# Kernel optimization log

Hardware: AMD Instinct MI355X
Metric: run time of the kernel (lower is better)

Reference implementation:

```python
import jax, jax.numpy as jnp
import numpy as np

B, S, D, H = 8, 512, 1024, 8
DPH = D // H            # 128, dim per head
MAX_REL = 32
NGRAM = 2               # 2-gram RNN on heads 4..7
NG_START, NG_COUNT = 4, 4
SCALE = float(DPH) ** 0.5


def setup_inputs() -> dict:
    key = jax.random.key(0)
    ks = jax.random.split(key, 12)
    w = lambda k, shp: jax.random.normal(k, shp, jnp.float32) * 0.02
    return {
        "x": jax.random.normal(ks[0], (B, S, D), jnp.float32),
        "mask": jax.random.randint(ks[1], (B, 1, S), 0, 2).astype(bool),
        "Wq": w(ks[2], (D, D)), "bq": jnp.zeros((D,), jnp.float32),
        "Wk": w(ks[3], (D, D)), "bk": jnp.zeros((D,), jnp.float32),
        "Wv": w(ks[4], (D, D)), "bv": jnp.zeros((D,), jnp.float32),
        "Wo": w(ks[5], (D, D)), "bo": jnp.zeros((D,), jnp.float32),
        "rel_emb": w(ks[6], (2 * MAX_REL + 1, DPH)),
        "Wih_f": w(ks[7], (DPH, DPH)), "Whh_f": w(ks[8], (DPH, DPH)),
        "bih_f": jnp.zeros((DPH,), jnp.float32), "bhh_f": jnp.zeros((DPH,), jnp.float32),
        "Wih_b": w(ks[9], (DPH, DPH)), "Whh_b": w(ks[10], (DPH, DPH)),
        "bih_b": jnp.zeros((DPH,), jnp.float32), "bhh_b": jnp.zeros((DPH,), jnp.float32),
    }


def reference(x, mask, Wq, bq, Wk, bk, Wv, bv, Wo, bo, rel_emb,
              Wih_f, Whh_f, bih_f, bhh_f, Wih_b, Whh_b, bih_b, bhh_b):
    shape_h = lambda t: t.reshape(B, S, H, DPH).transpose(0, 2, 1, 3)  # [B,H,S,d]
    q = shape_h(x @ Wq.T + bq)
    k = shape_h(x @ Wk.T + bk)
    v = shape_h(x @ Wv.T + bv)

    # --- ngram path: zero masked positions in q/k/v (all heads) ---
    m = mask[:, :, :, None]  # [B,1,S,1] broadcast over heads and d
    q = jnp.where(m, 0.0, q)
    k = jnp.where(m, 0.0, k)
    v = jnp.where(m, 0.0, v)

    # per-head 2-gram bidirectional RNN on heads NG_START..NG_START+NG_COUNT-1
    qh = q[:, NG_START:NG_START + NG_COUNT].reshape(-1, S, DPH)
    kh = k[:, NG_START:NG_START + NG_COUNT].reshape(-1, S, DPH)
    vh = v[:, NG_START:NG_START + NG_COUNT].reshape(-1, S, DPH)
    feats = jnp.concatenate([qh, kh, vh], axis=0)          # [3*B*NG_COUNT, S, d]
    shifted = jnp.pad(feats, ((0, 0), (1, 0), (0, 0)))[:, :-1]  # shift-by-1 (prev token)
    seq = jnp.stack([shifted, feats], axis=0).reshape(NGRAM, -1, DPH)  # [T, N*S, d]
    h0 = jnp.zeros((seq.shape[1], DPH), jnp.float32)
    fstep = lambda h, xt: (jnp.tanh(xt @ Wih_f.T + bih_f + h @ Whh_f.T + bhh_f), None)
    bstep = lambda h, xt: (jnp.tanh(xt @ Wih_b.T + bih_b + h @ Whh_b.T + bhh_b), None)
    hf, _ = jax.lax.scan(fstep, h0, seq)            # fwd final hidden
    hb, _ = jax.lax.scan(bstep, h0, seq[::-1])      # bwd final hidden
    yy = (hf + hb).reshape(3, B, NG_COUNT, S, DPH)  # sum of direction finals
    q = q.at[:, NG_START:NG_START + NG_COUNT].set(yy[0])
    k = k.at[:, NG_START:NG_START + NG_COUNT].set(yy[1])
    v = v.at[:, NG_START:NG_START + NG_COUNT].set(yy[2])

    # --- relative-position attention ---
    qs = q / SCALE
    r = jnp.arange(S)
    rel_idx = jnp.clip(r[None, :] - r[:, None], -MAX_REL, MAX_REL) + MAX_REL  # [S,S]
    rel_k = rel_emb[rel_idx]  # [S,S,d]; same table used for keys and values
    scores = jnp.einsum('bhqd,bhkd->bhqk', qs, k) + jnp.einsum('bhqd,qkd->bhqk', qs, rel_k)
    scores = jnp.where(mask[:, None], -1e18, scores)  # [B,1,1,S] broadcast
    attn = jax.nn.softmax(scores, axis=-1)
    ctx = jnp.einsum('bhqk,bhkd->bhqd', attn, v) + jnp.einsum('bhqk,qkd->bhqd', attn, rel_k)
    out = ctx.transpose(0, 2, 1, 3).reshape(B, S, D) @ Wo.T + bo
    return out, attn
```

## Files before the change

kernel.cpp:

```cpp
#include <hip/hip_runtime.h>


typedef __bf16 bf16x8 __attribute__((ext_vector_type(8)));
typedef float f32x4 __attribute__((ext_vector_type(4)));

#define MFMA16(a, b, c) __builtin_amdgcn_mfma_f32_16x16x32_bf16(a, b, c, 0, 0, 0)

__device__ __forceinline__ unsigned short f2bf(float f) {
  unsigned u = __float_as_uint(f);
  u += 0x7FFFu + ((u >> 16) & 1u);
  return (unsigned short)(u >> 16);
}
__device__ __forceinline__ uint2 pack4(float4 f) {
  uint2 r;
  r.x = (unsigned)f2bf(f.x) | ((unsigned)f2bf(f.y) << 16);
  r.y = (unsigned)f2bf(f.z) | ((unsigned)f2bf(f.w) << 16);
  return r;
}

__global__ __launch_bounds__(256) void prep_bf16(
    const float* __restrict__ x,
    const float* __restrict__ Wq, const float* __restrict__ Wk,
    const float* __restrict__ Wv, const float* __restrict__ Wo,
    const float* __restrict__ Wihf, const float* __restrict__ Whhf,
    const float* __restrict__ Wihb, const float* __restrict__ Whhb,
    unsigned short* __restrict__ xb, unsigned short* __restrict__ Wqkvb,
    unsigned short* __restrict__ Wob, unsigned short* __restrict__ Wrnnb) {
  int i = blockIdx.x * 256 + threadIdx.x;
  const float* src;
  unsigned short* dst;
  int off;
  if (i < 1048576) {
    src = x; dst = xb; off = i;
  } else if (i < 1310720) {
    src = Wq; dst = Wqkvb; off = i - 1048576;
  } else if (i < 1572864) {
    src = Wk; dst = Wqkvb + 1048576; off = i - 1310720;
  } else if (i < 1835008) {
    src = Wv; dst = Wqkvb + 2097152; off = i - 1572864;
  } else if (i < 2097152) {
    src = Wo; dst = Wob; off = i - 1835008;
  } else if (i < 2101248) {
    src = Wihf; dst = Wrnnb; off = i - 2097152;
  } else if (i < 2105344) {
    src = Whhf; dst = Wrnnb + 16384; off = i - 2101248;
  } else if (i < 2109440) {
    src = Wihb; dst = Wrnnb + 32768; off = i - 2105344;
  } else {
    src = Whhb; dst = Wrnnb + 49152; off = i - 2109440;
  }
  float4 f = *((const float4*)src + off);
  *(uint2*)(dst + (size_t)off * 4) = pack4(f);
}

__global__ __launch_bounds__(256) void qkv_proj(
    const unsigned short* __restrict__ xb, const unsigned short* __restrict__ Wqkvb,
    const float* __restrict__ bq, const float* __restrict__ bk,
    const float* __restrict__ bv, const int* __restrict__ mask,
    unsigned short* __restrict__ qb, unsigned short* __restrict__ kb,
    unsigned short* __restrict__ vb, unsigned short* __restrict__ vT) {
  __shared__ __align__(16) unsigned short As[128 * 72];
  __shared__ __align__(16) unsigned short Bs[128 * 72];
  const int bm = blockIdx.x & 31;
  const int bn = blockIdx.x >> 5;
  const int t = bn >> 3;
  const int nloc0 = (bn & 7) * 128;
  const unsigned short* W = Wqkvb + (size_t)t * 1048576;
  const float* bias = (t == 0) ? bq : (t == 1) ? bk : bv;
  const int tid = threadIdx.x;
  const int lane = tid & 63, w = tid >> 6;
  const int wm = (w >> 1) * 64, wn = (w & 1) * 64;
  const int lanelo = lane & 15, quad = lane >> 4;
  const int row0 = bm * 128;

  f32x4 acc[4][4];
  const f32x4 zf = {0.f, 0.f, 0.f, 0.f};
#pragma unroll
  for (int i = 0; i < 4; ++i)
#pragma unroll
    for (int j = 0; j < 4; ++j) acc[i][j] = zf;

  for (int kt = 0; kt < 16; ++kt) {
#pragma unroll
    for (int p = 0; p < 4; ++p) {
      int c = p * 256 + tid;
      int r = c >> 3, cc = c & 7;
      *(uint4*)(&As[r * 72 + cc * 8]) =
          *(const uint4*)(xb + (size_t)(row0 + r) * 1024 + kt * 64 + cc * 8);
      *(uint4*)(&Bs[r * 72 + cc * 8]) =
          *(const uint4*)(W + (size_t)(nloc0 + r) * 1024 + kt * 64 + cc * 8);
    }
    __syncthreads();
#pragma unroll
    for (int ks = 0; ks < 2; ++ks) {
      bf16x8 a[4], bb[4];
#pragma unroll
      for (int i = 0; i < 4; ++i)
        a[i] = *(const bf16x8*)(&As[(wm + i * 16 + lanelo) * 72 + ks * 32 + quad * 8]);
#pragma unroll
      for (int j = 0; j < 4; ++j)
        bb[j] = *(const bf16x8*)(&Bs[(wn + j * 16 + lanelo) * 72 + ks * 32 + quad * 8]);
#pragma unroll
      for (int i = 0; i < 4; ++i)
#pragma unroll
        for (int j = 0; j < 4; ++j) acc[i][j] = MFMA16(a[i], bb[j], acc[i][j]);
    }
    __syncthreads();
  }
#pragma unroll
  for (int i = 0; i < 4; ++i) {
#pragma unroll
    for (int j = 0; j < 4; ++j) {
      int jj = nloc0 + wn + j * 16 + lanelo;
      int hh = jj >> 7, dc = jj & 127;
      float bvv = bias[jj];
#pragma unroll
      for (int r = 0; r < 4; ++r) {
        int m = row0 + wm + i * 16 + quad * 4 + r;
        int b = m >> 9, s = m & 511;
        float val = acc[i][j][r] + bvv;
        if (mask[b * 512 + s]) val = 0.f;
        unsigned short o = f2bf(val);
        size_t off = ((size_t)(b * 8 + hh) * 512 + s) * 128 + dc;
        if (t == 0) qb[off] = o;
        else if (t == 1) kb[off] = o;
        else {
          vb[off] = o;
          vT[((size_t)(b * 8 + hh) * 128 + dc) * 512 + s] = o;
        }
      }
    }
  }
}

__global__ __launch_bounds__(256) void prep_rel(
    const float* __restrict__ rel, unsigned short* __restrict__ relb,
    unsigned short* __restrict__ relT) {
  int i = blockIdx.x * 256 + threadIdx.x;
  if (i < 65 * 128) relb[i] = f2bf(rel[i]);
  if (i < 128 * 96) {
    int d = i / 96, r = i - d * 96;
    relT[i] = (r < 65) ? f2bf(rel[r * 128 + d]) : (unsigned short)0;
  }
}

__global__ __launch_bounds__(256) void rnn_fused(
    const unsigned short* __restrict__ qb, const unsigned short* __restrict__ kb,
    const unsigned short* __restrict__ vb,
    const unsigned short* __restrict__ Wrnnb,
    const float* __restrict__ bihf, const float* __restrict__ bhhf,
    const float* __restrict__ bihb, const float* __restrict__ bhhb,
    unsigned short* __restrict__ rnn_out) {
  __shared__ __align__(16) unsigned short X[65 * 136];
  __shared__ __align__(16) unsigned short Wi[128 * 136];
  __shared__ __align__(16) unsigned short Wh[128 * 136];
  __shared__ __align__(16) unsigned short H1[64 * 136];
  __shared__ float cbf[128], cbb[128];

  const unsigned short* Wihfb = Wrnnb;
  const unsigned short* Whhfb = Wrnnb + 16384;
  const unsigned short* Wihbb = Wrnnb + 32768;
  const unsigned short* Whhbb = Wrnnb + 49152;

  const int gid = blockIdx.x;
  const int tile = gid & 7;
  const int g = gid >> 3;
  const int t = g >> 5;
  const int rem = g & 31;
  const int b = rem >> 2, h = (rem & 3) + 4;
  const int s0 = tile * 64;
  const unsigned short* src = (t == 0) ? qb : (t == 1) ? kb : vb;
  const size_t rowbase = (size_t)(b * 8 + h) * 512;
  const int tid = threadIdx.x;

  for (int c = tid; c < 65 * 16; c += 256) {
    int r = c >> 4, cc = c & 15;
    uint4 v4;
    if (r == 0 && s0 == 0) v4 = make_uint4(0, 0, 0, 0);
    else v4 = *(const uint4*)(src + (rowbase + (s0 - 1 + r)) * 128 + cc * 8);
    *(uint4*)(&X[r * 136 + cc * 8]) = v4;
  }
#pragma unroll
  for (int p = 0; p < 8; ++p) {
    int c = p * 256 + tid;
    int r = c >> 4, cc = c & 15;
    *(uint4*)(&Wi[r * 136 + cc * 8]) = *(const uint4*)(Wihfb + c * 8);
    *(uint4*)(&Wh[r * 136 + cc * 8]) = *(const uint4*)(Whhfb + c * 8);
  }
  if (tid < 128) {
    cbf[tid] = bihf[tid] + bhhf[tid];
    cbb[tid] = bihb[tid] + bhhb[tid];
  }
  __syncthreads();

  const int lane = tid & 63, w = tid >> 6;
  const int lanelo = lane & 15, quad = lane >> 4;
  const int marow = w * 16 + lanelo;
  const f32x4 zf = {0.f, 0.f, 0.f, 0.f};

  f32x4 g1[8];
#pragma unroll
  for (int j = 0; j < 8; ++j) g1[j] = zf;
#pragma unroll
  for (int ks = 0; ks < 4; ++ks) {
    bf16x8 a = *(const bf16x8*)(&X[marow * 136 + ks * 32 + quad * 8]);
#pragma unroll
    for (int j = 0; j < 8; ++j) {
      bf16x8 bb = *(const bf16x8*)(&Wi[(j * 16 + lanelo) * 136 + ks * 32 + quad * 8]);
      g1[j] = MFMA16(a, bb, g1[j]);
    }
  }
#pragma unroll
  for (int j = 0; j < 8; ++j) {
    int col = j * 16 + lanelo;
    float cb = cbf[col];
#pragma unroll
    for (int i = 0; i < 4; ++i) {
      int row = w * 16 + quad * 4 + i;
      H1[row * 136 + col] = f2bf(tanhf(g1[j][i] + cb));
    }
  }
  __syncthreads();
  f32x4 a2[8];
#pragma unroll
  for (int j = 0; j < 8; ++j) a2[j] = zf;
#pragma unroll
  for (int ks = 0; ks < 4; ++ks) {
    bf16x8 a = *(const bf16x8*)(&X[(marow + 1) * 136 + ks * 32 + quad * 8]);
#pragma unroll
    for (int j = 0; j < 8; ++j) {
      bf16x8 bb = *(const bf16x8*)(&Wi[(j * 16 + lanelo) * 136 + ks * 32 + quad * 8]);
      a2[j] = MFMA16(a, bb, a2[j]);
    }
  }
#pragma unroll
  for (int ks = 0; ks < 4; ++ks) {
    bf16x8 a = *(const bf16x8*)(&H1[marow * 136 + ks * 32 + quad * 8]);
#pragma unroll
    for (int j = 0; j < 8; ++j) {
      bf16x8 bb = *(const bf16x8*)(&Wh[(j * 16 + lanelo) * 136 + ks * 32 + quad * 8]);
      a2[j] = MFMA16(a, bb, a2[j]);
    }
  }
  float outF[8][4];
#pragma unroll
  for (int j = 0; j < 8; ++j) {
    int col = j * 16 + lanelo;
    float cb = cbf[col];
#pragma unroll
    for (int i = 0; i < 4; ++i) outF[j][i] = tanhf(a2[j][i] + cb);
  }
  __syncthreads();
#pragma unroll
  for (int p = 0; p < 8; ++p) {
    int c = p * 256 + tid;
    int r = c >> 4, cc = c & 15;
    *(uint4*)(&Wi[r * 136 + cc * 8]) = *(const uint4*)(Wihbb + c * 8);
    *(uint4*)(&Wh[r * 136 + cc * 8]) = *(const uint4*)(Whhbb + c * 8);
  }
  __syncthreads();
#pragma unroll
  for (int j = 0; j < 8; ++j) g1[j] = zf;
#pragma unroll
  for (int ks = 0; ks < 4; ++ks) {
    bf16x8 a = *(const bf16x8*)(&X[(marow + 1) * 136 + ks * 32 + quad * 8]);
#pragma unroll
    for (int j = 0; j < 8; ++j) {
      bf16x8 bb = *(const bf16x8*)(&Wi[(j * 16 + lanelo) * 136 + ks * 32 + quad * 8]);
      g1[j] = MFMA16(a, bb, g1[j]);
    }
  }
#pragma unroll
  for (int j = 0; j < 8; ++j) {
    int col = j * 16 + lanelo;
    float cb = cbb[col];
#pragma unroll
    for (int i = 0; i < 4; ++i) {
      int row = w * 16 + quad * 4 + i;
      H1[row * 136 + col] = f2bf(tanhf(g1[j][i] + cb));
    }
  }
  __syncthreads();
#pragma unroll
  for (int j = 0; j < 8; ++j) a2[j] = zf;
#pragma unroll
  for (int ks = 0; ks < 4; ++ks) {
    bf16x8 a = *(const bf16x8*)(&X[marow * 136 + ks * 32 + quad * 8]);
#pragma unroll
    for (int j = 0; j < 8; ++j) {
      bf16x8 bb = *(const bf16x8*)(&Wi[(j * 16 + lanelo) * 136 + ks * 32 + quad * 8]);
      a2[j] = MFMA16(a, bb, a2[j]);
    }
  }
#pragma unroll
  for (int ks = 0; ks < 4; ++ks) {
    bf16x8 a = *(const bf16x8*)(&H1[marow * 136 + ks * 32 + quad * 8]);
#pragma unroll
    for (int j = 0; j < 8; ++j) {
      bf16x8 bb = *(const bf16x8*)(&Wh[(j * 16 + lanelo) * 136 + ks * 32 + quad * 8]);
      a2[j] = MFMA16(a, bb, a2[j]);
    }
  }
#pragma unroll
  for (int j = 0; j < 8; ++j) {
    int col = j * 16 + lanelo;
    float cb = cbb[col];
#pragma unroll
    for (int i = 0; i < 4; ++i) {
      int row = w * 16 + quad * 4 + i;
      float val = outF[j][i] + tanhf(a2[j][i] + cb);
      rnn_out[((size_t)g * 512 + s0 + row) * 128 + col] = f2bf(val);
    }
  }
}

__global__ __launch_bounds__(256) void rnn_copyback(
    const unsigned short* __restrict__ rnn_out,
    unsigned short* __restrict__ qb, unsigned short* __restrict__ kb,
    unsigned short* __restrict__ vT) {
  int idx = blockIdx.x * 256 + threadIdx.x;
  int g = idx >> 16;
  int r2 = idx & 65535;
  int s = r2 >> 7, col = r2 & 127;
  int t = g >> 5, rem = g & 31, b = rem >> 2, h = (rem & 3) + 4;
  unsigned short val = rnn_out[idx];
  size_t off = ((size_t)(b * 8 + h) * 512 + s) * 128 + col;
  if (t == 0) qb[off] = val;
  else if (t == 1) kb[off] = val;
  else vT[((size_t)(b * 8 + h) * 128 + col) * 512 + s] = val;
}

__global__ __launch_bounds__(256) void scores_softmax(
    const unsigned short* __restrict__ qbuf, const unsigned short* __restrict__ kbuf,
    const unsigned short* __restrict__ relb, const int* __restrict__ mask,
    float* __restrict__ attn_out, unsigned short* __restrict__ abuf) {
  __shared__ __align__(16) unsigned short As[64 * 136];
  __shared__ __align__(16) unsigned short Bs[512 * 40];
  __shared__ float Ps[64 * 80];
  __shared__ float cmask[512];
  const int idx = blockIdx.x;
  const int qt = idx & 7, bh = idx >> 3, b = bh >> 3;
  const int q0 = qt * 64;
  const size_t qrow0 = (size_t)bh * 512 + q0;
  const int tid = threadIdx.x;

  for (int i = tid; i < 64 * 96; i += 256) abuf[qrow0 * 96 + i] = 0;
  for (int c = tid; c < 1024; c += 256) {
    int r = c >> 4, cc = c & 15;
    *(uint4*)(&As[r * 136 + cc * 8]) = *(const uint4*)(qbuf + (qrow0 + r) * 128 + cc * 8);
  }
  for (int i = tid; i < 512; i += 256) cmask[i] = mask[b * 512 + i] ? -1e9f : 0.f;
  __syncthreads();

  const int lane = tid & 63, w = tid >> 6;
  const int lanelo = lane & 15, quad = lane >> 4;
  const f32x4 zf = {0.f, 0.f, 0.f, 0.f};

  f32x4 pacc[5];
#pragma unroll
  for (int j = 0; j < 5; ++j) pacc[j] = zf;
  for (int ks = 0; ks < 4; ++ks) {
    for (int c = tid; c < 320; c += 256) {
      int r = c >> 2, cc = c & 3;
      uint4 v4 = (r < 65) ? *(const uint4*)(relb + r * 128 + ks * 32 + cc * 8)
                          : make_uint4(0, 0, 0, 0);
      *(uint4*)(&Bs[r * 40 + cc * 8]) = v4;
    }
    __syncthreads();
    bf16x8 a = *(const bf16x8*)(&As[(w * 16 + lanelo) * 136 + ks * 32 + quad * 8]);
#pragma unroll
    for (int j = 0; j < 5; ++j) {
      bf16x8 bb = *(const bf16x8*)(&Bs[(j * 16 + lanelo) * 40 + quad * 8]);
      pacc[j] = MFMA16(a, bb, pacc[j]);
    }
    __syncthreads();
  }
#pragma unroll
  for (int j = 0; j < 5; ++j) {
    int col = j * 16 + lanelo;
#pragma unroll
    for (int i = 0; i < 4; ++i) Ps[(w * 16 + quad * 4 + i) * 80 + col] = pacc[j][i];
  }
  __syncthreads();

  f32x4 acc[32];
#pragma unroll
  for (int j = 0; j < 32; ++j) acc[j] = zf;
  for (int ks = 0; ks < 4; ++ks) {
    for (int c = tid; c < 2048; c += 256) {
      int r = c >> 2, cc = c & 3;
      *(uint4*)(&Bs[r * 40 + cc * 8]) =
          *(const uint4*)(kbuf + ((size_t)bh * 512 + r) * 128 + ks * 32 + cc * 8);
    }
    __syncthreads();
    bf16x8 a = *(const bf16x8*)(&As[(w * 16 + lanelo) * 136 + ks * 32 + quad * 8]);
#pragma unroll
    for (int j = 0; j < 32; ++j) {
      bf16x8 bb = *(const bf16x8*)(&Bs[(j * 16 + lanelo) * 40 + quad * 8]);
      acc[j] = MFMA16(a, bb, acc[j]);
    }
    __syncthreads();
  }

  const float rscale = 0.08838834764831845f;
  float mrow[4] = {-1.0e30f, -1.0e30f, -1.0e30f, -1.0e30f};
#pragma unroll
  for (int j = 0; j < 32; ++j) {
    int k = j * 16 + lanelo;
    float cm = cmask[k];
#pragma unroll
    for (int i = 0; i < 4; ++i) {
      int row = w * 16 + quad * 4 + i;
      int qg = q0 + row;
      int d = k - qg;
      int r = min(max(d, -32), 32) + 32;
      float val = (acc[j][i] + Ps[row * 80 + r]) * rscale + cm;
      acc[j][i] = val;
      mrow[i] = fmaxf(mrow[i], val);
    }
  }
#pragma unroll
  for (int st = 1; st < 16; st <<= 1)
#pragma unroll
    for (int i = 0; i < 4; ++i) mrow[i] = fmaxf(mrow[i], __shfl_xor(mrow[i], st, 64));
  float srow[4] = {0.f, 0.f, 0.f, 0.f};
#pragma unroll
  for (int j = 0; j < 32; ++j)
#pragma unroll
    for (int i = 0; i < 4; ++i) {
      float e = __expf(acc[j][i] - mrow[i]);
      acc[j][i] = e;
      srow[i] += e;
    }
#pragma unroll
  for (int st = 1; st < 16; st <<= 1)
#pragma unroll
    for (int i = 0; i < 4; ++i) srow[i] += __shfl_xor(srow[i], st, 64);
  float rs[4];
#pragma unroll
  for (int i = 0; i < 4; ++i) rs[i] = (srow[i] > 0.f) ? 1.f / srow[i] : 0.f;

  float s0a[4] = {0.f, 0.f, 0.f, 0.f}, s64a[4] = {0.f, 0.f, 0.f, 0.f};
#pragma unroll
  for (int j = 0; j < 32; ++j) {
    int k = j * 16 + lanelo;
#pragma unroll
    for (int i = 0; i < 4; ++i) {
      int row = w * 16 + quad * 4 + i;
      int qg = q0 + row;
      float at = acc[j][i] * rs[i];
      attn_out[((size_t)bh * 512 + qg) * 512 + k] = at;
      int d = k - qg;
      if (d <= -32) s0a[i] += at;
      else if (d >= 32) s64a[i] += at;
      else abuf[((size_t)bh * 512 + qg) * 96 + (d + 32)] = f2bf(at);
    }
  }
#pragma unroll
  for (int st = 1; st < 16; st <<= 1)
#pragma unroll
    for (int i = 0; i < 4; ++i) {
      s0a[i] += __shfl_xor(s0a[i], st, 64);
      s64a[i] += __shfl_xor(s64a[i], st, 64);
    }
  if (lanelo == 0) {
#pragma unroll
    for (int i = 0; i < 4; ++i) {
      int qg = q0 + w * 16 + quad * 4 + i;
      abuf[((size_t)bh * 512 + qg) * 96 + 0] = f2bf(s0a[i]);
      abuf[((size_t)bh * 512 + qg) * 96 + 64] = f2bf(s64a[i]);
    }
  }
}

__global__ __launch_bounds__(256) void av_ctx(
    const float* __restrict__ attn, const unsigned short* __restrict__ abuf,
    const unsigned short* __restrict__ vT, const unsigned short* __restrict__ relT,
    unsigned short* __restrict__ ctx) {
  __shared__ __align__(16) unsigned short As[64 * 40];
  __shared__ __align__(16) unsigned short Bs[128 * 40];
  const int idx = blockIdx.x;
  const int qt = idx & 7, bh = idx >> 3;
  const int q0 = qt * 64;
  const int tid = threadIdx.x, lane = tid & 63, w = tid >> 6;
  const int lanelo = lane & 15, quad = lane >> 4;
  const f32x4 zf = {0.f, 0.f, 0.f, 0.f};
  f32x4 acc[8];
#pragma unroll
  for (int j = 0; j < 8; ++j) acc[j] = zf;

  for (int kt = 0; kt < 19; ++kt) {
    {
      int c = tid;
      int r = c >> 2, cc = c & 3;
      if (kt < 16) {
        const float* src = attn + ((size_t)bh * 512 + q0 + r) * 512 + kt * 32 + cc * 8;
        *(uint2*)(&As[r * 40 + cc * 8]) = pack4(*(const float4*)(src));
        *(uint2*)(&As[r * 40 + cc * 8 + 4]) = pack4(*(const float4*)(src + 4));
      } else {
        *(uint4*)(&As[r * 40 + cc * 8]) =
            *(const uint4*)(abuf + ((size_t)bh * 512 + q0 + r) * 96 + (kt - 16) * 32 + cc * 8);
      }
    }
#pragma unroll
    for (int p = 0; p < 2; ++p) {
      int c = p * 256 + tid;
      int r = c >> 2, cc = c & 3;
      uint4 vbv;
      if (kt < 16)
        vbv = *(const uint4*)(vT + ((size_t)bh * 128 + r) * 512 + kt * 32 + cc * 8);
      else
        vbv = *(const uint4*)(relT + r * 96 + (kt - 16) * 32 + cc * 8);
      *(uint4*)(&Bs[r * 40 + cc * 8]) = vbv;
    }
    __syncthreads();
    bf16x8 a = *(const bf16x8*)(&As[(w * 16 + lanelo) * 40 + quad * 8]);
#pragma unroll
    for (int j = 0; j < 8; ++j) {
      bf16x8 bb = *(const bf16x8*)(&Bs[(j * 16 + lanelo) * 40 + quad * 8]);
      acc[j] = MFMA16(a, bb, acc[j]);
    }
    __syncthreads();
  }
  const int b = bh >> 3, h = bh & 7;
#pragma unroll
  for (int j = 0; j < 8; ++j) {
    int d = j * 16 + lanelo;
#pragma unroll
    for (int i = 0; i < 4; ++i) {
      int qg = q0 + w * 16 + quad * 4 + i;
      ctx[((size_t)(b * 512 + qg)) * 1024 + h * 128 + d] = f2bf(acc[j][i]);
    }
  }
}

__global__ __launch_bounds__(256) void out_proj(
    const unsigned short* __restrict__ ctx, const unsigned short* __restrict__ Wob,
    const float* __restrict__ bo, float* __restrict__ outp) {
  __shared__ __align__(16) unsigned short As[128 * 72];
  __shared__ __align__(16) unsigned short Bs[128 * 72];
  const int bm = blockIdx.x & 31, bn = blockIdx.x >> 5;
  const int tid = threadIdx.x, lane = tid & 63, w = tid >> 6;
  const int wm = (w >> 1) * 64, wn = (w & 1) * 64;
  const int lanelo = lane & 15, quad = lane >> 4;
  const int row0 = bm * 128, col0 = bn * 128;
  f32x4 acc[4][4];
  const f32x4 zf = {0.f, 0.f, 0.f, 0.f};
#pragma unroll
  for (int i = 0; i < 4; ++i)
#pragma unroll
    for (int j = 0; j < 4; ++j) acc[i][j] = zf;

  for (int kt = 0; kt < 16; ++kt) {
#pragma unroll
    for (int p = 0; p < 4; ++p) {
      int c = p * 256 + tid;
      int r = c >> 3, cc = c & 7;
      *(uint4*)(&As[r * 72 + cc * 8]) =
          *(const uint4*)(ctx + (size_t)(row0 + r) * 1024 + kt * 64 + cc * 8);
      *(uint4*)(&Bs[r * 72 + cc * 8]) =
          *(const uint4*)(Wob + (size_t)(col0 + r) * 1024 + kt * 64 + cc * 8);
    }
    __syncthreads();
#pragma unroll
    for (int ks = 0; ks < 2; ++ks) {
      bf16x8 a[4], bb[4];
#pragma unroll
      for (int i = 0; i < 4; ++i)
        a[i] = *(const bf16x8*)(&As[(wm + i * 16 + lanelo) * 72 + ks * 32 + quad * 8]);
#pragma unroll
      for (int j = 0; j < 4; ++j)
        bb[j] = *(const bf16x8*)(&Bs[(wn + j * 16 + lanelo) * 72 + ks * 32 + quad * 8]);
#pragma unroll
      for (int i = 0; i < 4; ++i)
#pragma unroll
        for (int j = 0; j < 4; ++j) acc[i][j] = MFMA16(a[i], bb[j], acc[i][j]);
    }
    __syncthreads();
  }
#pragma unroll
  for (int i = 0; i < 4; ++i) {
#pragma unroll
    for (int j = 0; j < 4; ++j) {
      int n = col0 + wn + j * 16 + lanelo;
      float bbv = bo[n];
#pragma unroll
      for (int r = 0; r < 4; ++r) {
        int m = row0 + wm + i * 16 + quad * 4 + r;
        outp[(size_t)m * 1024 + n] = acc[i][j][r] + bbv;
      }
    }
  }
}

extern "C" void kernel_launch(void* const* d_in, const int* in_sizes, int n_in,
                              void* d_out, int out_size, void* d_ws, size_t ws_size,
                              hipStream_t stream) {
  const float* x    = (const float*)d_in[0];
  const int*   mask = (const int*)d_in[1];
  const float* Wq   = (const float*)d_in[2];
  const float* bq   = (const float*)d_in[3];
  const float* Wk   = (const float*)d_in[4];
  const float* bk   = (const float*)d_in[5];
  const float* Wv   = (const float*)d_in[6];
  const float* bv   = (const float*)d_in[7];
  const float* Wo   = (const float*)d_in[8];
  const float* bo   = (const float*)d_in[9];
  const float* rel  = (const float*)d_in[10];
  const float* Wihf = (const float*)d_in[11];
  const float* Whhf = (const float*)d_in[12];
  const float* bihf = (const float*)d_in[13];
  const float* bhhf = (const float*)d_in[14];
  const float* Wihb = (const float*)d_in[15];
  const float* Whhb = (const float*)d_in[16];
  const float* bihb = (const float*)d_in[17];
  const float* bhhb = (const float*)d_in[18];

  char* ws = (char*)d_ws;
  unsigned short* qb   = (unsigned short*)(ws + 0);
  unsigned short* kb   = (unsigned short*)(ws + 8388608);
  unsigned short* vT   = (unsigned short*)(ws + 16777216);
  unsigned short* abuf = (unsigned short*)(ws + 25165824);
  unsigned short* relb = (unsigned short*)(ws + 31457280);
  unsigned short* relT = (unsigned short*)(ws + 31473920);
  unsigned short* Wob  = (unsigned short*)(ws + 31498496);
  unsigned short* ctx  = qb;

  float* outp  = (float*)d_out;
  float* attnF = outp + 4194304;
  unsigned short* abase  = (unsigned short*)attnF;
  unsigned short* xb     = abase;
  unsigned short* vb     = abase + 4194304;
  unsigned short* rnnout = abase + 8388608;
  unsigned short* Wqkvb  = abase + 14680064;
  unsigned short* Wrnnb  = abase + 17825792;

  prep_bf16<<<dim3(8256), dim3(256), 0, stream>>>(
      x, Wq, Wk, Wv, Wo, Wihf, Whhf, Wihb, Whhb, xb, Wqkvb, Wob, Wrnnb);
  prep_rel<<<dim3(48), dim3(256), 0, stream>>>(rel, relb, relT);
  qkv_proj<<<dim3(768), dim3(256), 0, stream>>>(xb, Wqkvb, bq, bk, bv, mask,
                                                qb, kb, vb, vT);
  rnn_fused<<<dim3(768), dim3(256), 0, stream>>>(qb, kb, vb, Wrnnb,
                                                 bihf, bhhf, bihb, bhhb, rnnout);
  rnn_copyback<<<dim3(24576), dim3(256), 0, stream>>>(rnnout, qb, kb, vT);
  scores_softmax<<<dim3(512), dim3(256), 0, stream>>>(qb, kb, relb, mask, attnF, abuf);
  av_ctx<<<dim3(512), dim3(256), 0, stream>>>(attnF, abuf, vT, relT, ctx);
  out_proj<<<dim3(256), dim3(256), 0, stream>>>(ctx, Wob, bo, outp);
}
```

Baseline: 373.4 us.

## Load GEMM tiles directly into LDS with rotated-chunk swizzle instead of padding

Replaces the register-staged global-to-shared tile copies in the QKV projection, score, context and output-projection kernels with direct global_load_lds 16-byte loads. LDS rows drop their padding and use a rotated chunk index (XOR-like swizzle) to avoid bank conflicts on both the write and MFMA-read sides. The vT transpose store in the QKV epilogue is also packed into 8-byte writes of four consecutive sequence positions. This aims to cut VGPR pressure and load instruction overhead, but it depends on the per-wave LDS layout of the direct-load builtin being correct.

```diff
diff --git a/kernel.cpp b/kernel.cpp
--- a/kernel.cpp
+++ b/kernel.cpp
@@ -16,6 +16,11 @@
   r.x = (unsigned)f2bf(f.x) | ((unsigned)f2bf(f.y) << 16);
   r.y = (unsigned)f2bf(f.z) | ((unsigned)f2bf(f.w) << 16);
   return r;
+}
+__device__ __forceinline__ void gld16(const unsigned short* g, unsigned short* l) {
+  __builtin_amdgcn_global_load_lds(
+      (const __attribute__((address_space(1))) unsigned int*)g,
+      (__attribute__((address_space(3))) unsigned int*)l, 16, 0, 0);
 }
 
 __global__ __launch_bounds__(256) void prep_bf16(
@@ -59,8 +64,8 @@
     const float* __restrict__ bv, const int* __restrict__ mask,
     unsigned short* __restrict__ qb, unsigned short* __restrict__ kb,
     unsigned short* __restrict__ vb, unsigned short* __restrict__ vT) {
-  __shared__ __align__(16) unsigned short As[128 * 72];
-  __shared__ __align__(16) unsigned short Bs[128 * 72];
+  __shared__ __align__(16) unsigned short As[128 * 64];
+  __shared__ __align__(16) unsigned short Bs[128 * 64];
   const int bm = blockIdx.x & 31;
   const int bn = blockIdx.x >> 5;
   const int t = bn >> 3;
@@ -72,6 +77,8 @@
   const int wm = (w >> 1) * 64, wn = (w & 1) * 64;
   const int lanelo = lane & 15, quad = lane >> 4;
   const int row0 = bm * 128;
+  const int rloc = lane >> 3, pch = lane & 7;
+  const int lch = (pch - rloc) & 7;
 
   f32x4 acc[4][4];
   const f32x4 zf = {0.f, 0.f, 0.f, 0.f};
@@ -82,24 +89,23 @@
 
   for (int kt = 0; kt < 16; ++kt) {
 #pragma unroll
-    for (int p = 0; p < 4; ++p) {
-      int c = p * 256 + tid;
-      int r = c >> 3, cc = c & 7;
-      *(uint4*)(&As[r * 72 + cc * 8]) =
-          *(const uint4*)(xb + (size_t)(row0 + r) * 1024 + kt * 64 + cc * 8);
-      *(uint4*)(&Bs[r * 72 + cc * 8]) =
-          *(const uint4*)(W + (size_t)(nloc0 + r) * 1024 + kt * 64 + cc * 8);
+    for (int q = 0; q < 4; ++q) {
+      int seg = w * 4 + q;
+      int grow = seg * 8 + rloc;
+      gld16(xb + (size_t)(row0 + grow) * 1024 + kt * 64 + lch * 8, &As[seg * 512]);
+      gld16(W + (size_t)(nloc0 + grow) * 1024 + kt * 64 + lch * 8, &Bs[seg * 512]);
     }
     __syncthreads();
 #pragma unroll
     for (int ks = 0; ks < 2; ++ks) {
+      const int pA = (ks * 4 + quad + lanelo) & 7;
       bf16x8 a[4], bb[4];
 #pragma unroll
       for (int i = 0; i < 4; ++i)
-        a[i] = *(const bf16x8*)(&As[(wm + i * 16 + lanelo) * 72 + ks * 32 + quad * 8]);
+        a[i] = *(const bf16x8*)(&As[(wm + i * 16 + lanelo) * 64 + pA * 8]);
 #pragma unroll
       for (int j = 0; j < 4; ++j)
-        bb[j] = *(const bf16x8*)(&Bs[(wn + j * 16 + lanelo) * 72 + ks * 32 + quad * 8]);
+        bb[j] = *(const bf16x8*)(&Bs[(wn + j * 16 + lanelo) * 64 + pA * 8]);
 #pragma unroll
       for (int i = 0; i < 4; ++i)
 #pragma unroll
@@ -114,20 +120,26 @@
       int jj = nloc0 + wn + j * 16 + lanelo;
       int hh = jj >> 7, dc = jj & 127;
       float bvv = bias[jj];
+      int m0 = row0 + wm + i * 16 + quad * 4;
+      int b0 = m0 >> 9, sS = m0 & 511;
+      unsigned short ov[4];
 #pragma unroll
       for (int r = 0; r < 4; ++r) {
-        int m = row0 + wm + i * 16 + quad * 4 + r;
-        int b = m >> 9, s = m & 511;
+        int s = sS + r;
         float val = acc[i][j][r] + bvv;
-        if (mask[b * 512 + s]) val = 0.f;
+        if (mask[b0 * 512 + s]) val = 0.f;
         unsigned short o = f2bf(val);
-        size_t off = ((size_t)(b * 8 + hh) * 512 + s) * 128 + dc;
+        ov[r] = o;
+        size_t off = ((size_t)(b0 * 8 + hh) * 512 + s) * 128 + dc;
         if (t == 0) qb[off] = o;
         else if (t == 1) kb[off] = o;
-        else {
-          vb[off] = o;
-          vT[((size_t)(b * 8 + hh) * 128 + dc) * 512 + s] = o;
-        }
+        else vb[off] = o;
+      }
+      if (t == 2) {
+        uint2 pk;
+        pk.x = (unsigned)ov[0] | ((unsigned)ov[1] << 16);
+        pk.y = (unsigned)ov[2] | ((unsigned)ov[3] << 16);
+        *(uint2*)(&vT[((size_t)(b0 * 8 + hh) * 128 + dc) * 512 + sS]) = pk;
       }
     }
   }
@@ -335,7 +347,7 @@
     const unsigned short* __restrict__ relb, const int* __restrict__ mask,
     float* __restrict__ attn_out, unsigned short* __restrict__ abuf) {
   __shared__ __align__(16) unsigned short As[64 * 136];
-  __shared__ __align__(16) unsigned short Bs[512 * 40];
+  __shared__ __align__(16) unsigned short Bs[512 * 32];
   __shared__ float Ps[64 * 80];
   __shared__ float cmask[512];
   const int idx = blockIdx.x;
@@ -354,6 +366,9 @@
 
   const int lane = tid & 63, w = tid >> 6;
   const int lanelo = lane & 15, quad = lane >> 4;
+  const int rloc4 = lane >> 2, pch4 = lane & 3;
+  const int lch4 = (pch4 - rloc4) & 3;
+  const int pB = (quad + lanelo) & 3;
   const f32x4 zf = {0.f, 0.f, 0.f, 0.f};
 
   f32x4 pacc[5];
@@ -364,13 +379,13 @@
       int r = c >> 2, cc = c & 3;
       uint4 v4 = (r < 65) ? *(const uint4*)(relb + r * 128 + ks * 32 + cc * 8)
                           : make_uint4(0, 0, 0, 0);
-      *(uint4*)(&Bs[r * 40 + cc * 8]) = v4;
+      *(uint4*)(&Bs[r * 32 + ((cc + r) & 3) * 8]) = v4;
     }
     __syncthreads();
     bf16x8 a = *(const bf16x8*)(&As[(w * 16 + lanelo) * 136 + ks * 32 + quad * 8]);
 #pragma unroll
     for (int j = 0; j < 5; ++j) {
-      bf16x8 bb = *(const bf16x8*)(&Bs[(j * 16 + lanelo) * 40 + quad * 8]);
+      bf16x8 bb = *(const bf16x8*)(&Bs[(j * 16 + lanelo) * 32 + pB * 8]);
       pacc[j] = MFMA16(a, bb, pacc[j]);
     }
     __syncthreads();
@@ -387,16 +402,18 @@
 #pragma unroll
   for (int j = 0; j < 32; ++j) acc[j] = zf;
   for (int ks = 0; ks < 4; ++ks) {
-    for (int c = tid; c < 2048; c += 256) {
-      int r = c >> 2, cc = c & 3;
-      *(uint4*)(&Bs[r * 40 + cc * 8]) =
-          *(const uint4*)(kbuf + ((size_t)bh * 512 + r) * 128 + ks * 32 + cc * 8);
+#pragma unroll
+    for (int q = 0; q < 8; ++q) {
+      int seg = w * 8 + q;
+      int grow = seg * 16 + rloc4;
+      gld16(kbuf + ((size_t)bh * 512 + grow) * 128 + ks * 32 + lch4 * 8,
+            &Bs[seg * 512]);
     }
     __syncthreads();
     bf16x8 a = *(const bf16x8*)(&As[(w * 16 + lanelo) * 136 + ks * 32 + quad * 8]);
 #pragma unroll
     for (int j = 0; j < 32; ++j) {
-      bf16x8 bb = *(const bf16x8*)(&Bs[(j * 16 + lanelo) * 40 + quad * 8]);
+      bf16x8 bb = *(const bf16x8*)(&Bs[(j * 16 + lanelo) * 32 + pB * 8]);
       acc[j] = MFMA16(a, bb, acc[j]);
     }
     __syncthreads();
@@ -478,12 +495,15 @@
     const unsigned short* __restrict__ vT, const unsigned short* __restrict__ relT,
     unsigned short* __restrict__ ctx) {
   __shared__ __align__(16) unsigned short As[64 * 40];
-  __shared__ __align__(16) unsigned short Bs[128 * 40];
+  __shared__ __align__(16) unsigned short Bs[128 * 32];
   const int idx = blockIdx.x;
   const int qt = idx & 7, bh = idx >> 3;
   const int q0 = qt * 64;
   const int tid = threadIdx.x, lane = tid & 63, w = tid >> 6;
   const int lanelo = lane & 15, quad = lane >> 4;
+  const int rloc4 = lane >> 2, pch4 = lane & 3;
+  const int lch4 = (pch4 - rloc4) & 3;
+  const int pB = (quad + lanelo) & 3;
   const f32x4 zf = {0.f, 0.f, 0.f, 0.f};
   f32x4 acc[8];
 #pragma unroll
@@ -503,21 +523,19 @@
       }
     }
 #pragma unroll
-    for (int p = 0; p < 2; ++p) {
-      int c = p * 256 + tid;
-      int r = c >> 2, cc = c & 3;
-      uint4 vbv;
+    for (int q = 0; q < 2; ++q) {
+      int seg = w * 2 + q;
+      int grow = seg * 16 + rloc4;
       if (kt < 16)
-        vbv = *(const uint4*)(vT + ((size_t)bh * 128 + r) * 512 + kt * 32 + cc * 8);
+        gld16(vT + ((size_t)bh * 128 + grow) * 512 + kt * 32 + lch4 * 8, &Bs[seg * 512]);
       else
-        vbv = *(const uint4*)(relT + r * 96 + (kt - 16) * 32 + cc * 8);
-      *(uint4*)(&Bs[r * 40 + cc * 8]) = vbv;
+        gld16(relT + grow * 96 + (kt - 16) * 32 + lch4 * 8, &Bs[seg * 512]);
     }
     __syncthreads();
     bf16x8 a = *(const bf16x8*)(&As[(w * 16 + lanelo) * 40 + quad * 8]);
 #pragma unroll
     for (int j = 0; j < 8; ++j) {
-      bf16x8 bb = *(const bf16x8*)(&Bs[(j * 16 + lanelo) * 40 + quad * 8]);
+      bf16x8 bb = *(const bf16x8*)(&Bs[(j * 16 + lanelo) * 32 + pB * 8]);
       acc[j] = MFMA16(a, bb, acc[j]);
     }
     __syncthreads();
@@ -537,13 +555,15 @@
 __global__ __launch_bounds__(256) void out_proj(
     const unsigned short* __restrict__ ctx, const unsigned short* __restrict__ Wob,
     const float* __restrict__ bo, float* __restrict__ outp) {
-  __shared__ __align__(16) unsigned short As[128 * 72];
-  __shared__ __align__(16) unsigned short Bs[128 * 72];
+  __shared__ __align__(16) unsigned short As[128 * 64];
+  __shared__ __align__(16) unsigned short Bs[128 * 64];
   const int bm = blockIdx.x & 31, bn = blockIdx.x >> 5;
   const int tid = threadIdx.x, lane = tid & 63, w = tid >> 6;
   const int wm = (w >> 1) * 64, wn = (w & 1) * 64;
   const int lanelo = lane & 15, quad = lane >> 4;
   const int row0 = bm * 128, col0 = bn * 128;
+  const int rloc = lane >> 3, pch = lane & 7;
+  const int lch = (pch - rloc) & 7;
   f32x4 acc[4][4];
   const f32x4 zf = {0.f, 0.f, 0.f, 0.f};
 #pragma unroll
@@ -553,24 +573,23 @@
 
   for (int kt = 0; kt < 16; ++kt) {
 #pragma unroll
-    for (int p = 0; p < 4; ++p) {
-      int c = p * 256 + tid;
-      int r = c >> 3, cc = c & 7;
-      *(uint4*)(&As[r * 72 + cc * 8]) =
-          *(const uint4*)(ctx + (size_t)(row0 + r) * 1024 + kt * 64 + cc * 8);
-      *(uint4*)(&Bs[r * 72 + cc * 8]) =
-          *(const uint4*)(Wob + (size_t)(col0 + r) * 1024 + kt * 64 + cc * 8);
+    for (int q = 0; q < 4; ++q) {
+      int seg = w * 4 + q;
+      int grow = seg * 8 + rloc;
+      gld16(ctx + (size_t)(row0 + grow) * 1024 + kt * 64 + lch * 8, &As[seg * 512]);
+      gld16(Wob + (size_t)(col0 + grow) * 1024 + kt * 64 + lch * 8, &Bs[seg * 512]);
     }
     __syncthreads();
 #pragma unroll
     for (int ks = 0; ks < 2; ++ks) {
+      const int pA = (ks * 4 + quad + lanelo) & 7;
       bf16x8 a[4], bb[4];
 #pragma unroll
       for (int i = 0; i < 4; ++i)
-        a[i] = *(const bf16x8*)(&As[(wm + i * 16 + lanelo) * 72 + ks * 32 + quad * 8]);
+        a[i] = *(const bf16x8*)(&As[(wm + i * 16 + lanelo) * 64 + pA * 8]);
 #pragma unroll
       for (int j = 0; j < 4; ++j)
-        bb[j] = *(const bf16x8*)(&Bs[(wn + j * 16 + lanelo) * 72 + ks * 32 + quad * 8]);
+        bb[j] = *(const bf16x8*)(&Bs[(wn + j * 16 + lanelo) * 64 + pA * 8]);
 #pragma unroll
       for (int i = 0; i < 4; ++i)
 #pragma unroll
```

Result: faster. 355.5 us (-4.8%).
